# Kernel optimization log

Measured on AMD Instinct MI355X. Metric: run time of the kernel, lower is better.

Reference implementation:

```python
import jax, jax.numpy as jnp
import numpy as np
import math

V, D, H, L, F, S, B = 32000, 1024, 16, 4, 4096, 1024, 2
DK = D // H
EPS = 1e-5


def _pe(seq_len, d_model):
    pos = jnp.arange(seq_len, dtype=jnp.float32)[:, None]
    div = jnp.exp(jnp.arange(0, d_model, 2, dtype=jnp.float32) * (-math.log(10000.0) / d_model))
    ang = pos * div  # [S, D/2]
    return jnp.stack([jnp.sin(ang), jnp.cos(ang)], axis=-1).reshape(seq_len, d_model)


def _ln(x, g, b):
    m = jnp.mean(x, axis=-1, keepdims=True)
    v = jnp.mean(jnp.square(x - m), axis=-1, keepdims=True)
    return (x - m) * jax.lax.rsqrt(v + EPS) * g + b


def setup_inputs() -> dict:
    key = jax.random.key(0)
    ks = jax.random.split(key, 12)
    std = 0.02
    inp = {
        "input_ids": jax.random.randint(ks[0], (B, S), 0, V, dtype=jnp.int32),
        "embed": std * jax.random.normal(ks[1], (V, D), dtype=jnp.float32),
        "Wq": std * jax.random.normal(ks[2], (L, D, D), dtype=jnp.float32),
        "bq": jnp.zeros((L, D), jnp.float32),
        "Wk": std * jax.random.normal(ks[3], (L, D, D), dtype=jnp.float32),
        "bk": jnp.zeros((L, D), jnp.float32),
        "Wv": std * jax.random.normal(ks[4], (L, D, D), dtype=jnp.float32),
        "bv": jnp.zeros((L, D), jnp.float32),
        "Wo": std * jax.random.normal(ks[5], (L, D, D), dtype=jnp.float32),
        "bo": jnp.zeros((L, D), jnp.float32),
        "ln1_g": jnp.ones((L, D), jnp.float32), "ln1_b": jnp.zeros((L, D), jnp.float32),
        "W1": std * jax.random.normal(ks[6], (L, F, D), dtype=jnp.float32),
        "b1": jnp.zeros((L, F), jnp.float32),
        "W2": std * jax.random.normal(ks[7], (L, D, F), dtype=jnp.float32),
        "b2": jnp.zeros((L, D), jnp.float32),
        "ln2_g": jnp.ones((L, D), jnp.float32), "ln2_b": jnp.zeros((L, D), jnp.float32),
        "lnf_g": jnp.ones((D,), jnp.float32), "lnf_b": jnp.zeros((D,), jnp.float32),
        "head_w": std * jax.random.normal(ks[8], (V, D), dtype=jnp.float32),
    }
    return inp


def _forward(input_ids, embed, Wq, bq, Wk, bk, Wv, bv, Wo, bo,
             ln1_g, ln1_b, W1, b1, W2, b2, ln2_g, ln2_b, lnf_g, lnf_b, head_w):
    b, s = input_ids.shape
    x = embed[input_ids] * jnp.float32(math.sqrt(D))  # [B,S,D]
    x = x + _pe(s, D)[None, :, :]
    causal = jnp.tril(jnp.ones((s, s), dtype=bool))  # [S,S]
    scale = jnp.float32(1.0 / math.sqrt(DK))
    for l in range(L):
        q = (x @ Wq[l].T + bq[l]).reshape(b, s, H, DK).transpose(0, 2, 1, 3)
        k = (x @ Wk[l].T + bk[l]).reshape(b, s, H, DK).transpose(0, 2, 1, 3)
        v = (x @ Wv[l].T + bv[l]).reshape(b, s, H, DK).transpose(0, 2, 1, 3)
        scores = jnp.einsum('bhqd,bhkd->bhqk', q, k) * scale
        scores = jnp.where(causal[None, None], scores, jnp.float32(-1e9))
        attn = jax.nn.softmax(scores, axis=-1)
        o = jnp.einsum('bhqk,bhkd->bhqd', attn, v).transpose(0, 2, 1, 3).reshape(b, s, D)
        o = o @ Wo[l].T + bo[l]
        x = _ln(x + o, ln1_g[l], ln1_b[l])
        ff = jax.nn.relu(x @ W1[l].T + b1[l]) @ W2[l].T + b2[l]
        x = _ln(x + ff, ln2_g[l], ln2_b[l])
    x = _ln(x, lnf_g, lnf_b)
    return x @ head_w.T  # logits [B,S,V]


def reference(input_ids, embed, Wq, bq, Wk, bk, Wv, bv, Wo, bo,
              ln1_g, ln1_b, W1, b1, W2, b2, ln2_g, ln2_b, lnf_g, lnf_b, head_w):
    return _forward(input_ids, embed, Wq, bq, Wk, bk, Wv, bv, Wo, bo,
                    ln1_g, ln1_b, W1, b1, W2, b2, ln2_g, ln2_b, lnf_g, lnf_b, head_w)
```

## Files before the change

kernel.cpp:

```cpp
#include <hip/hip_runtime.h>
#include <math.h>


namespace {
constexpr int kV  = 32000;
constexpr int kD  = 1024;
constexpr int kH  = 16;
constexpr int kL  = 4;
constexpr int kF  = 4096;
constexpr int kS  = 1024;
constexpr int kB  = 2;
constexpr int kDK = 64;
constexpr int kM  = kB * kS;
constexpr float kEps   = 1e-5f;
constexpr float kScale = 0.125f;
}

using short8 = __attribute__((ext_vector_type(8))) short;
using f32x4  = __attribute__((ext_vector_type(4))) float;

__device__ __forceinline__ unsigned short f2bf(float f) {
  union { float f; unsigned int u; } x{f};
  const unsigned int r = x.u + 0x7fffu + ((x.u >> 16) & 1u);
  return (unsigned short)(r >> 16);
}

__device__ __forceinline__ void llds16(const void* g, void* l) {
  __builtin_amdgcn_global_load_lds(
      (const __attribute__((address_space(1))) unsigned int*)g,
      (__attribute__((address_space(3))) unsigned int*)l, 16, 0, 0);
}

__device__ __forceinline__ float block_sum256(float v, float* scratch) {
#pragma unroll
  for (int off = 32; off > 0; off >>= 1) v += __shfl_down(v, off, 64);
  const int wid  = threadIdx.x >> 6;
  const int lane = threadIdx.x & 63;
  __syncthreads();
  if (lane == 0) scratch[wid] = v;
  __syncthreads();
  return scratch[0] + scratch[1] + scratch[2] + scratch[3];
}

__global__ __launch_bounds__(256) void f2bf_kernel(const float* __restrict__ in,
                                                   unsigned short* __restrict__ out,
                                                   int n4) {
  const int i = blockIdx.x * 256 + threadIdx.x;
  if (i < n4) {
    const float4 v = ((const float4*)in)[i];
    ushort4 o;
    o.x = f2bf(v.x); o.y = f2bf(v.y); o.z = f2bf(v.z); o.w = f2bf(v.w);
    ((ushort4*)out)[i] = o;
  }
}

__global__ __launch_bounds__(256) void f2bf_layer_kernel(
    const float* __restrict__ wq, const float* __restrict__ wk,
    const float* __restrict__ wv, const float* __restrict__ wo,
    const float* __restrict__ w1, const float* __restrict__ w2,
    unsigned short* __restrict__ dst) {
  const int i = blockIdx.x * 256 + threadIdx.x;
  const float* src;
  size_t so, doff;
  if (i < 1048576) {
    const int seg = i >> 18;
    const int off = i & 262143;
    src = (seg == 0) ? wq : (seg == 1) ? wk : (seg == 2) ? wv : wo;
    so = off;
    doff = (size_t)seg * 1048576 + (size_t)off * 4;
  } else {
    const int j = i - 1048576;
    if (j < 1048576) { src = w1; so = j; doff = 4194304 + (size_t)j * 4; }
    else             { src = w2; so = j - 1048576; doff = 8388608 + (size_t)(j - 1048576) * 4; }
  }
  const float4 v = ((const float4*)src)[so];
  ushort4 o;
  o.x = f2bf(v.x); o.y = f2bf(v.y); o.z = f2bf(v.z); o.w = f2bf(v.w);
  *(ushort4*)(dst + doff) = o;
}

__global__ __launch_bounds__(256) void embed_pe_kernel(
    const int* __restrict__ ids, const float* __restrict__ embed,
    float* __restrict__ x, unsigned short* __restrict__ xb) {
  const int row = blockIdx.x;
  const int s   = row & (kS - 1);
  const int id  = ids[row];
  const float* erow = embed + (size_t)id * kD;
#pragma unroll
  for (int i = 0; i < kD / 256; ++i) {
    const int d = threadIdx.x + i * 256;
    const int p = d >> 1;
    const float div = expf((float)p * -0.017988946039015984f);
    const float ang = (float)s * div;
    const float pe  = (d & 1) ? cosf(ang) : sinf(ang);
    const float v = erow[d] * 32.0f + pe;
    x[(size_t)row * kD + d]  = v;
    xb[(size_t)row * kD + d] = f2bf(v);
  }
}

template <int MODE>
__device__ __forceinline__ void gemm_core(int bm, int bn,
                                          const unsigned short* __restrict__ A,
                                          const unsigned short* __restrict__ W,
                                          const float* __restrict__ bias,
                                          void* __restrict__ Cout,
                                          int M, int N, int K,
                                          int k0begin, int k0end, float oscale) {
  __shared__ __align__(16) unsigned short As[128 * 32];
  __shared__ __align__(16) unsigned short Ws[128 * 32];
  const int t    = threadIdx.x;
  const int lane = t & 63;
  const int w    = t >> 6;
  const int wm   = (w >> 1) * 64;
  const int wn   = (w & 1) * 64;
  const int l15  = lane & 15;
  const int quad = lane >> 4;

  f32x4 acc[4][4] = {};

  for (int k0 = k0begin; k0 < k0end; k0 += 32) {
    __syncthreads();
#pragma unroll
    for (int i = 0; i < 2; ++i) {
      const int e   = i * 256 + t;
      const int row = e >> 2;
      const int kc  = (e & 3) * 8;
      const int ldsoff = (i * 256 + w * 64) * 8;
      llds16(A + (size_t)(bm + row) * K + k0 + kc, &As[ldsoff]);
      llds16(W + (size_t)(bn + row) * K + k0 + kc, &Ws[ldsoff]);
    }
    __syncthreads();
    short8 af[4], bf[4];
#pragma unroll
    for (int i = 0; i < 4; ++i)
      af[i] = *(const short8*)&As[(wm + i * 16 + l15) * 32 + quad * 8];
#pragma unroll
    for (int j = 0; j < 4; ++j)
      bf[j] = *(const short8*)&Ws[(wn + j * 16 + l15) * 32 + quad * 8];
#pragma unroll
    for (int i = 0; i < 4; ++i)
#pragma unroll
      for (int j = 0; j < 4; ++j)
        acc[i][j] = __builtin_amdgcn_mfma_f32_16x16x32_bf16(af[i], bf[j], acc[i][j], 0, 0, 0);
  }

#pragma unroll
  for (int i = 0; i < 4; ++i) {
#pragma unroll
    for (int r = 0; r < 4; ++r) {
      const int m = bm + wm + i * 16 + quad * 4 + r;
#pragma unroll
      for (int j = 0; j < 4; ++j) {
        const int n = bn + wn + j * 16 + l15;
        float v = acc[i][j][r] + (bias ? bias[n] : 0.0f);
        if (MODE == 2) v = fmaxf(v, 0.0f);
        if (MODE == 0) {
          ((float*)Cout)[(size_t)m * N + n] = v;
        } else if (MODE == 1) {
          const int b = m >> 10, s = m & 1023;
          const int h = n >> 6,  dk = n & 63;
          ((unsigned short*)Cout)[((size_t)(b * kH + h) * kS + s) * kDK + dk] = f2bf(v * oscale);
        } else if (MODE == 3) {
          const int b = m >> 10, s = m & 1023;
          const int h = n >> 6,  dk = n & 63;
          ((unsigned short*)Cout)[((size_t)(b * kH + h) * kDK + dk) * kS + s] = f2bf(v);
        } else {
          ((unsigned short*)Cout)[(size_t)m * N + n] = f2bf(v);
        }
      }
    }
  }
}

__global__ __launch_bounds__(256) void gemm_head_kernel(
    const unsigned short* __restrict__ A, const unsigned short* __restrict__ W,
    float* __restrict__ C) {
  const int bid = blockIdx.x;
  const int wg  = (bid & 7) * 500 + (bid >> 3);
  const int bm  = (wg & 15) * 128;
  const int bn  = (wg >> 4) * 128;
  gemm_core<0>(bm, bn, A, W, nullptr, C, kM, kV, kD, 0, kD, 1.0f);
}

__global__ __launch_bounds__(256) void gemm_qkv_kernel(
    const unsigned short* __restrict__ A,
    const unsigned short* __restrict__ wq, const unsigned short* __restrict__ wk,
    const unsigned short* __restrict__ wv,
    const float* __restrict__ bq_, const float* __restrict__ bk_,
    const float* __restrict__ bv_,
    unsigned short* __restrict__ qo, unsigned short* __restrict__ ko,
    unsigned short* __restrict__ vo) {
  const int bm = blockIdx.y * 128;
  const int bn = blockIdx.x * 128;
  const int z  = blockIdx.z;
  if (z == 0) {
    gemm_core<1>(bm, bn, A, wq, bq_, qo, kM, kD, kD, 0, kD, kScale);
  } else if (z == 1) {
    gemm_core<1>(bm, bn, A, wk, bk_, ko, kM, kD, kD, 0, kD, 1.0f);
  } else {
    gemm_core<3>(bm, bn, A, wv, bv_, vo, kM, kD, kD, 0, kD, 1.0f);
  }
}

__global__ __launch_bounds__(256) void gemm_splitk_kernel(
    const unsigned short* __restrict__ A, const unsigned short* __restrict__ W,
    const float* __restrict__ bias, float* __restrict__ C0,
    float* __restrict__ C1, int M, int N, int K) {
  const int bm = blockIdx.y * 128;
  const int bn = blockIdx.x * 128;
  if (blockIdx.z == 0)
    gemm_core<0>(bm, bn, A, W, bias, C0, M, N, K, 0, K / 2, 1.0f);
  else
    gemm_core<0>(bm, bn, A, W, nullptr, C1, M, N, K, K / 2, K, 1.0f);
}

__global__ __launch_bounds__(256) void gemm_bf16relu_kernel(
    const unsigned short* __restrict__ A, const unsigned short* __restrict__ W,
    const float* __restrict__ bias, unsigned short* __restrict__ C,
    int M, int N, int K) {
  gemm_core<2>(blockIdx.y * 128, blockIdx.x * 128, A, W, bias, C, M, N, K, 0, K, 1.0f);
}

__global__ __launch_bounds__(256) void attn_mfma_kernel(
    const unsigned short* __restrict__ q, const unsigned short* __restrict__ k,
    const unsigned short* __restrict__ vt, unsigned short* __restrict__ ob) {
  const int bid = blockIdx.x;
  const int wg  = (bid & 7) * 64 + (bid >> 3);
  const int qt  = wg & 15;
  const int h   = (wg >> 4) & 15;
  const int b   = wg >> 8;
  const int q0  = qt * 64;

  __shared__ __align__(16) unsigned short Ps[4][16 * 64];

  const int t    = threadIdx.x;
  const int lane = t & 63;
  const int w    = t >> 6;
  const int l15  = lane & 15;
  const int quad = lane >> 4;

  const size_t base = (size_t)(b * kH + h) * kS * kDK;

  short8 aq[2];
#pragma unroll
  for (int ks = 0; ks < 2; ++ks)
    aq[ks] = *(const short8*)(q + base + (size_t)(q0 + w * 16 + l15) * kDK + ks * 32 + quad * 8);

  f32x4 acc_o[4] = {};
  float m[4]    = {-1e30f, -1e30f, -1e30f, -1e30f};
  float lsum[4] = {0.f, 0.f, 0.f, 0.f};

  for (int kt = 0; kt <= qt; ++kt) {
    f32x4 s[4] = {};
#pragma unroll
    for (int j = 0; j < 4; ++j) {
#pragma unroll
      for (int ks = 0; ks < 2; ++ks) {
        const short8 bk8 = *(const short8*)(k + base +
            (size_t)(kt * 64 + j * 16 + l15) * kDK + ks * 32 + quad * 8);
        s[j] = __builtin_amdgcn_mfma_f32_16x16x32_bf16(aq[ks], bk8, s[j], 0, 0, 0);
      }
    }

    if (kt == qt) {
      const int rb = w * 16 + quad * 4;
#pragma unroll
      for (int j = 0; j < 4; ++j) {
        const int kg = j * 16 + l15;
#pragma unroll
        for (int r = 0; r < 4; ++r)
          if (kg > rb + r) s[j][r] = -1e30f;
      }
    }

    float pm[4];
#pragma unroll
    for (int r = 0; r < 4; ++r)
      pm[r] = fmaxf(fmaxf(s[0][r], s[1][r]), fmaxf(s[2][r], s[3][r]));
#pragma unroll
    for (int off = 8; off > 0; off >>= 1)
#pragma unroll
      for (int r = 0; r < 4; ++r)
        pm[r] = fmaxf(pm[r], __shfl_xor(pm[r], off, 64));

    float alpha[4];
#pragma unroll
    for (int r = 0; r < 4; ++r) {
      const float mn = fmaxf(m[r], pm[r]);
      alpha[r] = __expf(m[r] - mn);
      m[r] = mn;
    }

    float rs[4] = {0.f, 0.f, 0.f, 0.f};
    unsigned short pb16[4][4];
#pragma unroll
    for (int j = 0; j < 4; ++j)
#pragma unroll
      for (int r = 0; r < 4; ++r) {
        const float e = __expf(s[j][r] - m[r]);
        rs[r] += e;
        pb16[j][r] = f2bf(e);
      }
#pragma unroll
    for (int off = 8; off > 0; off >>= 1)
#pragma unroll
      for (int r = 0; r < 4; ++r)
        rs[r] += __shfl_xor(rs[r], off, 64);
#pragma unroll
    for (int r = 0; r < 4; ++r) lsum[r] = lsum[r] * alpha[r] + rs[r];
#pragma unroll
    for (int jd = 0; jd < 4; ++jd)
#pragma unroll
      for (int r = 0; r < 4; ++r) acc_o[jd][r] *= alpha[r];

#pragma unroll
    for (int j = 0; j < 4; ++j)
#pragma unroll
      for (int r = 0; r < 4; ++r) {
        const int row = quad * 4 + r;
        const int col = j * 16 + l15;
        Ps[w][row * 64 + (((col >> 3) ^ (row & 7)) << 3) + (col & 7)] = pb16[j][r];
      }
    asm volatile("s_waitcnt lgkmcnt(0)" ::: "memory");
    __builtin_amdgcn_sched_barrier(0);

    short8 ap[2];
#pragma unroll
    for (int ks = 0; ks < 2; ++ks)
      ap[ks] = *(const short8*)&Ps[w][l15 * 64 + (((ks * 4 + quad) ^ (l15 & 7)) * 8)];

#pragma unroll
    for (int jd = 0; jd < 4; ++jd) {
#pragma unroll
      for (int ks = 0; ks < 2; ++ks) {
        const short8 bv8 = *(const short8*)(vt + base +
            (size_t)(jd * 16 + l15) * kS + kt * 64 + ks * 32 + quad * 8);
        acc_o[jd] = __builtin_amdgcn_mfma_f32_16x16x32_bf16(ap[ks], bv8, acc_o[jd], 0, 0, 0);
      }
    }
  }

  float inv[4];
#pragma unroll
  for (int r = 0; r < 4; ++r) inv[r] = 1.0f / lsum[r];
#pragma unroll
  for (int jd = 0; jd < 4; ++jd)
#pragma unroll
    for (int r = 0; r < 4; ++r) {
      const int qg = q0 + w * 16 + quad * 4 + r;
      ob[(size_t)(b * kS + qg) * kD + h * kDK + jd * 16 + l15] =
          f2bf(acc_o[jd][r] * inv[r]);
    }
}

__global__ __launch_bounds__(256) void add_ln_kernel(
    float* __restrict__ x, const float* __restrict__ res,
    const float* __restrict__ res2,
    const float* __restrict__ g, const float* __restrict__ bta,
    unsigned short* __restrict__ xb) {
  const int row = blockIdx.x;
  const int t   = threadIdx.x;
  __shared__ float scratch[4];
  float vals[4];
  float sum = 0.f;
  float* xrow = x + (size_t)row * kD;
#pragma unroll
  for (int i = 0; i < 4; ++i) {
    const int d = t + i * 256;
    float vv = xrow[d];
    if (res)  vv += res[(size_t)row * kD + d];
    if (res2) vv += res2[(size_t)row * kD + d];
    vals[i] = vv;
    sum += vv;
  }
  const float mean = block_sum256(sum, scratch) * (1.0f / kD);
  float vsum = 0.f;
#pragma unroll
  for (int i = 0; i < 4; ++i) {
    const float dd = vals[i] - mean;
    vsum += dd * dd;
  }
  const float var  = block_sum256(vsum, scratch) * (1.0f / kD);
  const float rstd = rsqrtf(var + kEps);
#pragma unroll
  for (int i = 0; i < 4; ++i) {
    const int d = t + i * 256;
    const float o = (vals[i] - mean) * rstd * g[d] + bta[d];
    xrow[d] = o;
    xb[(size_t)row * kD + d] = f2bf(o);
  }
}

extern "C" void kernel_launch(void* const* d_in, const int* in_sizes, int n_in,
                              void* d_out, int out_size, void* d_ws, size_t ws_size,
                              hipStream_t stream) {
  const int*   ids   = (const int*)  d_in[0];
  const float* embed = (const float*)d_in[1];
  const float* Wq    = (const float*)d_in[2];
  const float* bq    = (const float*)d_in[3];
  const float* Wk    = (const float*)d_in[4];
  const float* bk    = (const float*)d_in[5];
  const float* Wv    = (const float*)d_in[6];
  const float* bv    = (const float*)d_in[7];
  const float* Wo    = (const float*)d_in[8];
  const float* bo    = (const float*)d_in[9];
  const float* ln1g  = (const float*)d_in[10];
  const float* ln1b  = (const float*)d_in[11];
  const float* W1    = (const float*)d_in[12];
  const float* b1    = (const float*)d_in[13];
  const float* W2    = (const float*)d_in[14];
  const float* b2    = (const float*)d_in[15];
  const float* ln2g  = (const float*)d_in[16];
  const float* ln2b  = (const float*)d_in[17];
  const float* lnfg  = (const float*)d_in[18];
  const float* lnfb  = (const float*)d_in[19];
  const float* headw = (const float*)d_in[20];

  char* ws = (char*)d_ws;
  float*          x    = (float*)          (ws);
  unsigned short* xb   = (unsigned short*) (ws + 8388608);
  unsigned short* qbb  = (unsigned short*) (ws + 12582912);
  unsigned short* kbb  = (unsigned short*) (ws + 16777216);
  unsigned short* vtb  = (unsigned short*) (ws + 20971520);
  unsigned short* ob   = (unsigned short*) (ws + 25165824);
  unsigned short* ff1b = (unsigned short*) (ws + 29360128);
  float*          pb   = (float*)          (ws + 46137344);
  float*          pb2  = (float*)          (ws + 54525952);
  unsigned short* wbuf = (unsigned short*) (ws + 67108864);

  const dim3 blk(256);
  embed_pe_kernel<<<kM, blk, 0, stream>>>(ids, embed, x, xb);

  for (int l = 0; l < kL; ++l) {
    const size_t oD = (size_t)l * kD * kD;
    const size_t oF = (size_t)l * kF * kD;
    f2bf_layer_kernel<<<12288, blk, 0, stream>>>(
        Wq + oD, Wk + oD, Wv + oD, Wo + oD, W1 + oF, W2 + oF, wbuf);

    gemm_qkv_kernel<<<dim3(8, 16, 3), blk, 0, stream>>>(
        xb, wbuf, wbuf + 1048576, wbuf + 2097152,
        bq + (size_t)l * kD, bk + (size_t)l * kD, bv + (size_t)l * kD,
        qbb, kbb, vtb);
    attn_mfma_kernel<<<kB * kH * (kS / 64), blk, 0, stream>>>(qbb, kbb, vtb, ob);
    gemm_splitk_kernel<<<dim3(8, 16, 2), blk, 0, stream>>>(
        ob, wbuf + 3145728, bo + (size_t)l * kD, pb, pb2, kM, kD, kD);
    add_ln_kernel<<<kM, blk, 0, stream>>>(
        x, pb, pb2, ln1g + (size_t)l * kD, ln1b + (size_t)l * kD, xb);
    gemm_bf16relu_kernel<<<dim3(32, 16), blk, 0, stream>>>(
        xb, wbuf + 4194304, b1 + (size_t)l * kF, ff1b, kM, kF, kD);
    gemm_splitk_kernel<<<dim3(8, 16, 2), blk, 0, stream>>>(
        ff1b, wbuf + 8388608, b2 + (size_t)l * kD, pb, pb2, kM, kD, kF);
    add_ln_kernel<<<kM, blk, 0, stream>>>(
        x, pb, pb2, ln2g + (size_t)l * kD, ln2b + (size_t)l * kD, xb);
  }

  add_ln_kernel<<<kM, blk, 0, stream>>>(x, nullptr, nullptr, lnfg, lnfb, xb);
  f2bf_kernel<<<32000, blk, 0, stream>>>(headw, wbuf, 8192000);
  gemm_head_kernel<<<dim3(4000), blk, 0, stream>>>(xb, wbuf, (float*)d_out);
}
```

Measured before the change: 1.651 ms.

## Double-buffer K/V tiles in LDS for attention and compute PE in double

The attention kernel now stages each 64-row K tile and V^T tile into swizzled, double-buffered shared memory using direct global-to-LDS loads. The next tile is prefetched while the current one is consumed, and a block barrier is added per iteration. Previously each wave read K and V straight from global memory with no reuse across the four waves, so the change aims to cut redundant global traffic and hide load latency. Separately, the positional-encoding computation switches to double-precision exp/sin/cos, which looks like an accuracy fix and adds a small cost to the embedding kernel.

```diff
diff --git a/kernel.cpp b/kernel.cpp
--- a/kernel.cpp
+++ b/kernel.cpp
@@ -90,9 +90,9 @@
   for (int i = 0; i < kD / 256; ++i) {
     const int d = threadIdx.x + i * 256;
     const int p = d >> 1;
-    const float div = expf((float)p * -0.017988946039015984f);
-    const float ang = (float)s * div;
-    const float pe  = (d & 1) ? cosf(ang) : sinf(ang);
+    const double div = exp((double)(2 * p) * (-9.210340371976184 / 1024.0));
+    const double ang = (double)s * div;
+    const float pe = (d & 1) ? (float)cos(ang) : (float)sin(ang);
     const float v = erow[d] * 32.0f + pe;
     x[(size_t)row * kD + d]  = v;
     xb[(size_t)row * kD + d] = f2bf(v);
@@ -232,6 +232,8 @@
   const int b   = wg >> 8;
   const int q0  = qt * 64;
 
+  __shared__ __align__(16) unsigned short Ks[2][64 * 64];
+  __shared__ __align__(16) unsigned short Vs[2][64 * 64];
   __shared__ __align__(16) unsigned short Ps[4][16 * 64];
 
   const int t    = threadIdx.x;
@@ -242,6 +244,19 @@
 
   const size_t base = (size_t)(b * kH + h) * kS * kDK;
 
+  auto stage = [&](int kt_, int buf) {
+#pragma unroll
+    for (int i = 0; i < 2; ++i) {
+      const int e   = i * 256 + t;
+      const int row = e >> 3;
+      const int g   = e & 7;
+      llds16(k + base + (size_t)(kt_ * 64 + row) * kDK + ((g ^ (row & 7)) * 8),
+             &Ks[buf][(i * 256 + w * 64) * 8]);
+      llds16(vt + base + (size_t)row * kS + kt_ * 64 + ((g ^ (row & 7)) * 8),
+             &Vs[buf][(i * 256 + w * 64) * 8]);
+    }
+  };
+
   short8 aq[2];
 #pragma unroll
   for (int ks = 0; ks < 2; ++ks)
@@ -251,14 +266,20 @@
   float m[4]    = {-1e30f, -1e30f, -1e30f, -1e30f};
   float lsum[4] = {0.f, 0.f, 0.f, 0.f};
 
+  stage(0, 0);
+  __syncthreads();
+
   for (int kt = 0; kt <= qt; ++kt) {
+    const int cur = kt & 1;
+    if (kt < qt) stage(kt + 1, cur ^ 1);
+
     f32x4 s[4] = {};
 #pragma unroll
     for (int j = 0; j < 4; ++j) {
 #pragma unroll
       for (int ks = 0; ks < 2; ++ks) {
-        const short8 bk8 = *(const short8*)(k + base +
-            (size_t)(kt * 64 + j * 16 + l15) * kDK + ks * 32 + quad * 8);
+        const short8 bk8 = *(const short8*)&Ks[cur][(j * 16 + l15) * 64 +
+                                                   (((ks * 4 + quad) ^ (l15 & 7)) * 8)];
         s[j] = __builtin_amdgcn_mfma_f32_16x16x32_bf16(aq[ks], bk8, s[j], 0, 0, 0);
       }
     }
@@ -334,11 +355,13 @@
     for (int jd = 0; jd < 4; ++jd) {
 #pragma unroll
       for (int ks = 0; ks < 2; ++ks) {
-        const short8 bv8 = *(const short8*)(vt + base +
-            (size_t)(jd * 16 + l15) * kS + kt * 64 + ks * 32 + quad * 8);
+        const short8 bv8 = *(const short8*)&Vs[cur][(jd * 16 + l15) * 64 +
+                                                   (((ks * 4 + quad) ^ (l15 & 7)) * 8)];
         acc_o[jd] = __builtin_amdgcn_mfma_f32_16x16x32_bf16(ap[ks], bv8, acc_o[jd], 0, 0, 0);
       }
     }
+
+    __syncthreads();
   }
 
   float inv[4];
```

New measurement: 1.533 ms. 7.2% less time.
